# Kernel tuning notes

Measured on AMD Instinct MI355X. Metric: run time of the kernel, lower is better.

Reference implementation:

```python
import jax, jax.numpy as jnp
import numpy as np

D = 2048
N = 16384
ETA = 0.01


def setup_inputs() -> dict:
    key = jax.random.key(0)
    k_theta, k_xs = jax.random.split(key)
    theta = jax.random.normal(k_theta, (D,), dtype=jnp.float32)
    # per-layer params x_k, init uniform(-1/sqrt(d), 1/sqrt(d)) as in torch module
    stdv = 1.0 / np.sqrt(D)
    xs = jax.random.uniform(k_xs, (N, D), dtype=jnp.float32, minval=-stdv, maxval=stdv)
    return {"theta": theta, "xs": xs}


def reference(theta, xs):
    # Each layer: pred = <x, theta>; grad = -x / (1 + exp(pred));
    # theta_next = theta - eta * grad = theta + eta * x / (1 + exp(pred)).
    def step(th, x):
        pred = jnp.dot(x, th)
        th_next = th + ETA * x / (1.0 + jnp.exp(pred))
        return th_next, None

    theta_out, _ = jax.lax.scan(step, theta, xs)
    return theta_out
```

## Files before the change

kernel.cpp:

```cpp
#include <hip/hip_runtime.h>
#include <hip/hip_bf16.h>
#include <stdint.h>

#define D_DIM 2048
#define N_STEPS 16384
#define B_BLK 1024
#define N_BLK (N_STEPS / B_BLK)
#define T_P (B_BLK / 128)
#define N_TILE (T_P * (T_P + 1) / 2)
#define ETA 0.01f
#define NWG 256
#define FLAG_STRIDE 16
#define FLAG_INTS (NWG * FLAG_STRIDE + 16)

typedef __attribute__((ext_vector_type(8))) short short8_t;
typedef __attribute__((ext_vector_type(4))) float floatx4;

__device__ __forceinline__ short f2bf(float f) {
  __hip_bfloat16 h = __float2bfloat16(f);
  return __builtin_bit_cast(short, h);
}
__device__ __forceinline__ float bf2f(uint32_t bits) {
  return __builtin_bit_cast(float, bits << 16);
}

__device__ __forceinline__ void store_wt(float* p, float v) {
  __hip_atomic_store(p, v, __ATOMIC_RELAXED, __HIP_MEMORY_SCOPE_AGENT);
}

__device__ __forceinline__ void gl_lds16(const short* g, short* l) {
  __builtin_amdgcn_global_load_lds(
      (const __attribute__((address_space(1))) void*)g,
      (__attribute__((address_space(3))) void*)l, 16, 0, 0);
}

__global__ __launch_bounds__(256) void cast_kernel(
    const float* __restrict__ xs, short* __restrict__ xb,
    const float* __restrict__ theta_in, float* __restrict__ theta_arr,
    int* __restrict__ flags) {
  size_t i = (size_t)blockIdx.x * 256 + threadIdx.x;
  float4 a = ((const float4*)xs)[i * 2];
  float4 b = ((const float4*)xs)[i * 2 + 1];
  short8_t v;
  v[0] = f2bf(a.x); v[1] = f2bf(a.y); v[2] = f2bf(a.z); v[3] = f2bf(a.w);
  v[4] = f2bf(b.x); v[5] = f2bf(b.y); v[6] = f2bf(b.z); v[7] = f2bf(b.w);
  *(short8_t*)(xb + i * 8) = v;

  if (blockIdx.x == 0) {
    int tid = threadIdx.x;
    for (int k = tid; k < FLAG_INTS; k += 256) flags[k] = 0;
    float4 t0 = ((const float4*)theta_in)[tid * 2];
    float4 t1 = ((const float4*)theta_in)[tid * 2 + 1];
    ((float4*)theta_arr)[tid * 2] = t0;
    ((float4*)theta_arr)[tid * 2 + 1] = t1;
  }
}

__global__ __launch_bounds__(256) void gram_kernel(const short* __restrict__ xb,
                                                   short* __restrict__ G) {
  int i = blockIdx.x;
  int x = i & 7, j = i >> 3;
  int b = (j < 36) ? x : x + 8;
  int t = (j < 36) ? j : j - 36;
  int ti = 0;
  while ((ti + 1) * (ti + 2) / 2 <= t) ti++;
  int tj = t - ti * (ti + 1) / 2;

  __shared__ short As[128 * 64];
  __shared__ short Bs[128 * 64];

  int tid = threadIdx.x;
  int lane = tid & 63;
  int w = tid >> 6;
  int wm = w >> 1, wn = w & 1;
  int quad = lane >> 4, rr = lane & 15;

  floatx4 acc[4][4];
#pragma unroll
  for (int ii = 0; ii < 4; ii++)
#pragma unroll
    for (int jj = 0; jj < 4; jj++)
#pragma unroll
      for (int r = 0; r < 4; r++) acc[ii][jj][r] = 0.f;

  const short* Arow = xb + (size_t)(b * B_BLK + ti * 128) * D_DIM;
  const short* Brow = xb + (size_t)(b * B_BLK + tj * 128) * D_DIM;
  bool diag = (ti == tj);

  for (int kk = 0; kk < D_DIM; kk += 64) {
#pragma unroll
    for (int tch = 0; tch < 4; tch++) {
      int chunk = tch * 256 + tid;
      int row = chunk >> 3, slot = chunk & 7;
      int cc = slot ^ (row & 7);
      gl_lds16(Arow + (size_t)row * D_DIM + kk + cc * 8, &As[chunk * 8]);
      if (!diag)
        gl_lds16(Brow + (size_t)row * D_DIM + kk + cc * 8, &Bs[chunk * 8]);
    }
    __syncthreads();

    const short* Bsrc = diag ? As : Bs;
#pragma unroll
    for (int ks = 0; ks < 2; ks++) {
      short8_t af[4], bfr[4];
#pragma unroll
      for (int mt = 0; mt < 4; mt++) {
        int r = wm * 64 + mt * 16 + rr;
        int slot = (ks * 4 + quad) ^ (r & 7);
        af[mt] = *(const short8_t*)(&As[r * 64 + slot * 8]);
      }
#pragma unroll
      for (int nt = 0; nt < 4; nt++) {
        int r = wn * 64 + nt * 16 + rr;
        int slot = (ks * 4 + quad) ^ (r & 7);
        bfr[nt] = *(const short8_t*)(&Bsrc[r * 64 + slot * 8]);
      }
#pragma unroll
      for (int mt = 0; mt < 4; mt++)
#pragma unroll
        for (int nt = 0; nt < 4; nt++)
          acc[mt][nt] = __builtin_amdgcn_mfma_f32_16x16x32_bf16(
              af[mt], bfr[nt], acc[mt][nt], 0, 0, 0);
    }
    __syncthreads();
  }

  size_t gbase = ((size_t)(b * N_TILE + t)) * (128 * 128);
  int col0 = lane & 15;
  int row0 = (lane >> 4) * 4;
#pragma unroll
  for (int mt = 0; mt < 4; mt++)
#pragma unroll
    for (int nt = 0; nt < 4; nt++)
#pragma unroll
      for (int r = 0; r < 4; r++) {
        int row = wm * 64 + mt * 16 + row0 + r;
        int col = wn * 64 + nt * 16 + col0;
        G[gbase + (size_t)row * 128 + col] = f2bf(acc[mt][nt][r]);
      }
}

__device__ __forceinline__ void bar_arrive(int* flags, int wg, int tid,
                                           int gen) {
  __syncthreads();
  if (tid == 0)
    __hip_atomic_store(&flags[wg * FLAG_STRIDE], gen, __ATOMIC_RELAXED,
                       __HIP_MEMORY_SCOPE_AGENT);
}

__device__ __forceinline__ void bar_wait(int* flags, int tid, int gen) {
  int guard = 0;
  while (__hip_atomic_load(&flags[tid * FLAG_STRIDE], __ATOMIC_RELAXED,
                           __HIP_MEMORY_SCOPE_AGENT) < gen &&
         guard < (1 << 20)) {
    guard++;
    __builtin_amdgcn_s_sleep(1);
  }
  asm volatile("" ::: "memory");
  __syncthreads();
}

__device__ __forceinline__ float wave_reduce(float s) {
  for (int off = 32; off; off >>= 1) s += __shfl_xor(s, off, 64);
  return s;
}

__global__ __launch_bounds__(256, 1) void solve_kernel(
    const short* __restrict__ xb, const short* __restrict__ G,
    float* __restrict__ theta_arr, float* __restrict__ c0_arr,
    float* __restrict__ c1_arr, int* flags, float* __restrict__ d_out) {
  int tid = threadIdx.x;
  int wg = blockIdx.x;
  int lane = tid & 63;
  int wid = tid >> 6;
  int gw = wg * 4 + wid;
  int ti = gw >> 7, kr = gw & 127;
  int oct = (wg & 7) * 32 + (wg >> 3);
  int d0 = oct * 8;
  int gen = 0;

  __shared__ float redc[4][8];

  short8_t xa[4];
  uint32_t gv[8];
  short8_t xc[4];

  {
    const short* xr = xb + (size_t)gw * D_DIM;
#pragma unroll
    for (int i = 0; i < 4; i++)
      xa[i] = *(const short8_t*)(xr + (i * 64 + lane) * 8);
#pragma unroll
    for (int tj = 0; tj < T_P; tj++)
      if (tj <= ti) {
        size_t base = ((size_t)(ti * (ti + 1) / 2 + tj)) * (128 * 128) +
                      (size_t)kr * 128;
        gv[tj] = *(const uint32_t*)(G + base + lane * 2);
      }
  }

  for (int b = 0; b < N_BLK; b++) {
    const float* theta = theta_arr + (size_t)b * D_DIM;
    float* c0 = c0_arr + (size_t)b * B_BLK;
    float* c1 = c1_arr + (size_t)b * B_BLK;
    float p_k;
    float th8 = 0.f;

    {
      if (tid < 8) th8 = theta[d0 + tid];
      float s = 0.f;
#pragma unroll
      for (int i = 0; i < 4; i++) {
        int idx = (i * 64 + lane) * 8;
        float4 t0 = *(const float4*)(theta + idx);
        float4 t1 = *(const float4*)(theta + idx + 4);
        short8_t xv = xa[i];
        s += bf2f((uint16_t)xv[0]) * t0.x + bf2f((uint16_t)xv[1]) * t0.y +
             bf2f((uint16_t)xv[2]) * t0.z + bf2f((uint16_t)xv[3]) * t0.w +
             bf2f((uint16_t)xv[4]) * t1.x + bf2f((uint16_t)xv[5]) * t1.y +
             bf2f((uint16_t)xv[6]) * t1.z + bf2f((uint16_t)xv[7]) * t1.w;
      }
      s = wave_reduce(s);
      p_k = s;
      if (lane == 0) store_wt(&c0[gw], ETA / (1.f + __expf(s)));
    }
    bar_arrive(flags, wg, tid, ++gen);
    {
      const short* xp = xb + ((size_t)b * B_BLK + tid * 4) * D_DIM + d0;
#pragma unroll
      for (int j = 0; j < 4; j++)
        xc[j] = *(const short8_t*)(xp + (size_t)j * D_DIM);
    }
    bar_wait(flags, tid, gen);

    {
      float2 cv[T_P];
#pragma unroll
      for (int tj = 0; tj < T_P; tj++)
        if (tj <= ti) cv[tj] = *(const float2*)(c0 + tj * 128 + lane * 2);
      float s = 0.f;
      int jc = lane * 2;
#pragma unroll
      for (int tj = 0; tj < T_P; tj++)
        if (tj <= ti) {
          int lim = (tj == ti) ? kr : 128;
          if (jc < lim) s += bf2f(gv[tj] & 0xffffu) * cv[tj].x;
          if (jc + 1 < lim) s += bf2f(gv[tj] >> 16) * cv[tj].y;
        }
      s = wave_reduce(s);
      if (lane == 0) store_wt(&c1[gw], ETA / (1.f + __expf(p_k + s)));
    }
    bar_arrive(flags, wg, tid, ++gen);
    if (b + 1 < N_BLK) {
      const short* xr = xb + (size_t)((b + 1) * B_BLK + gw) * D_DIM;
#pragma unroll
      for (int i = 0; i < 4; i++)
        xa[i] = *(const short8_t*)(xr + (i * 64 + lane) * 8);
    }
    bar_wait(flags, tid, gen);

    {
      float4 c1v = *(const float4*)(c1 + tid * 4);
      float a8[8];
#pragma unroll
      for (int jj = 0; jj < 8; jj++) a8[jj] = 0.f;
#pragma unroll
      for (int j = 0; j < 4; j++) {
        float c = (&c1v.x)[j];
        short8_t xv = xc[j];
#pragma unroll
        for (int jj = 0; jj < 8; jj++) a8[jj] += c * bf2f((uint16_t)xv[jj]);
      }
#pragma unroll
      for (int off = 32; off; off >>= 1)
#pragma unroll
        for (int jj = 0; jj < 8; jj++) a8[jj] += __shfl_xor(a8[jj], off, 64);
      if (lane == 0) {
#pragma unroll
        for (int jj = 0; jj < 8; jj++) redc[wid][jj] = a8[jj];
      }
      __syncthreads();
      if (tid < 8) {
        float tot =
            redc[0][tid] + redc[1][tid] + redc[2][tid] + redc[3][tid];
        float* dst = (b + 1 < N_BLK)
                         ? &theta_arr[(size_t)(b + 1) * D_DIM + d0 + tid]
                         : &d_out[d0 + tid];
        store_wt(dst, th8 + tot);
      }
    }
    if (b + 1 < N_BLK) {
      bar_arrive(flags, wg, tid, ++gen);
      {
        size_t base =
            ((size_t)((b + 1) * N_TILE + ti * (ti + 1) / 2)) * (128 * 128) +
            (size_t)kr * 128;
#pragma unroll
        for (int tj = 0; tj < T_P; tj++)
          if (tj <= ti)
            gv[tj] = *(const uint32_t*)(G + base + (size_t)tj * (128 * 128) +
                                        lane * 2);
      }
      bar_wait(flags, tid, gen);
    }
  }
}

extern "C" void kernel_launch(void* const* d_in, const int* in_sizes, int n_in,
                              void* d_out, int out_size, void* d_ws,
                              size_t ws_size, hipStream_t stream) {
  const float* theta_in = (const float*)d_in[0];
  const float* xs = (const float*)d_in[1];

  char* ws = (char*)d_ws;
  const size_t XB_BYTES = (size_t)N_STEPS * D_DIM * sizeof(short);
  const size_t G_BYTES = (size_t)N_BLK * N_TILE * 128 * 128 * sizeof(short);
  short* xb = (short*)ws;
  short* G = (short*)(ws + XB_BYTES);
  float* theta_arr = (float*)(ws + XB_BYTES + G_BYTES);
  float* c0_arr = theta_arr + (size_t)(N_BLK + 1) * D_DIM;
  float* c1_arr = c0_arr + (size_t)N_BLK * B_BLK;
  int* flags = (int*)(c1_arr + (size_t)N_BLK * B_BLK);

  cast_kernel<<<(N_STEPS * D_DIM / 8) / 256, 256, 0, stream>>>(
      xs, xb, theta_in, theta_arr, flags);
  gram_kernel<<<N_BLK * N_TILE, 256, 0, stream>>>(xb, G);
  solve_kernel<<<NWG, 256, 0, stream>>>(xb, G, theta_arr, c0_arr, c1_arr,
                                        flags, (float*)d_out);
}
```

Measured before the change: 350.7 us.

## Fuse cast and Gram into one prep kernel with per-block readiness counters

The separate cast and Gram kernels are merged into a single prep kernel. Cast workgroups (one per row) write bf16 rows and bump a per-block counter, and Gram workgroups spin until their block's rows are ready, so Gram work can overlap the cast instead of waiting for a full kernel boundary. Flag initialisation moves to a hipMemsetAsync. The solve kernel is split into two launches over halves of the blocks, with the barrier generation carried across. This relies on cast workgroups being scheduled ahead of the spinning Gram workgroups and adds an extra launch and a memset.

```diff
diff --git a/kernel.cpp b/kernel.cpp
--- a/kernel.cpp
+++ b/kernel.cpp
@@ -12,9 +12,13 @@
 #define NWG 256
 #define FLAG_STRIDE 16
 #define FLAG_INTS (NWG * FLAG_STRIDE + 16)
+#define GRAM_WGS (N_BLK * N_TILE)
+#define CAST_WGS N_STEPS
+#define PREP_WGS (GRAM_WGS + CAST_WGS)
 
 typedef __attribute__((ext_vector_type(8))) short short8_t;
 typedef __attribute__((ext_vector_type(4))) float floatx4;
+typedef __attribute__((ext_vector_type(2))) unsigned long long ulong2_t;
 
 __device__ __forceinline__ short f2bf(float f) {
   __hip_bfloat16 h = __float2bfloat16(f);
@@ -25,6 +29,9 @@
 }
 
 __device__ __forceinline__ void store_wt(float* p, float v) {
+  __hip_atomic_store(p, v, __ATOMIC_RELAXED, __HIP_MEMORY_SCOPE_AGENT);
+}
+__device__ __forceinline__ void store_wt64(uint64_t* p, uint64_t v) {
   __hip_atomic_store(p, v, __ATOMIC_RELAXED, __HIP_MEMORY_SCOPE_AGENT);
 }
 
@@ -34,42 +41,58 @@
       (__attribute__((address_space(3))) void*)l, 16, 0, 0);
 }
 
-__global__ __launch_bounds__(256) void cast_kernel(
-    const float* __restrict__ xs, short* __restrict__ xb,
+__global__ __launch_bounds__(256) void prep_kernel(
+    const float* __restrict__ xs, short* xb, short* __restrict__ G,
     const float* __restrict__ theta_in, float* __restrict__ theta_arr,
-    int* __restrict__ flags) {
-  size_t i = (size_t)blockIdx.x * 256 + threadIdx.x;
-  float4 a = ((const float4*)xs)[i * 2];
-  float4 b = ((const float4*)xs)[i * 2 + 1];
-  short8_t v;
-  v[0] = f2bf(a.x); v[1] = f2bf(a.y); v[2] = f2bf(a.z); v[3] = f2bf(a.w);
-  v[4] = f2bf(b.x); v[5] = f2bf(b.y); v[6] = f2bf(b.z); v[7] = f2bf(b.w);
-  *(short8_t*)(xb + i * 8) = v;
-
-  if (blockIdx.x == 0) {
-    int tid = threadIdx.x;
-    for (int k = tid; k < FLAG_INTS; k += 256) flags[k] = 0;
-    float4 t0 = ((const float4*)theta_in)[tid * 2];
-    float4 t1 = ((const float4*)theta_in)[tid * 2 + 1];
-    ((float4*)theta_arr)[tid * 2] = t0;
-    ((float4*)theta_arr)[tid * 2 + 1] = t1;
-  }
-}
-
-__global__ __launch_bounds__(256) void gram_kernel(const short* __restrict__ xb,
-                                                   short* __restrict__ G) {
-  int i = blockIdx.x;
-  int x = i & 7, j = i >> 3;
-  int b = (j < 36) ? x : x + 8;
-  int t = (j < 36) ? j : j - 36;
+    int* castcnt) {
+  int tid = threadIdx.x;
+  int wg = blockIdx.x;
+
+  __shared__ short As[128 * 64];
+  __shared__ short Bs[128 * 64];
+
+  if (wg >= GRAM_WGS) {
+    int r = wg - GRAM_WGS;
+    const float* src = xs + (size_t)r * D_DIM + tid * 8;
+    float4 a = *(const float4*)(src);
+    float4 bq = *(const float4*)(src + 4);
+    short8_t v;
+    v[0] = f2bf(a.x); v[1] = f2bf(a.y); v[2] = f2bf(a.z); v[3] = f2bf(a.w);
+    v[4] = f2bf(bq.x); v[5] = f2bf(bq.y); v[6] = f2bf(bq.z); v[7] = f2bf(bq.w);
+    ulong2_t u = __builtin_bit_cast(ulong2_t, v);
+    uint64_t* dst = (uint64_t*)(xb + (size_t)r * D_DIM + tid * 8);
+    store_wt64(dst, u[0]);
+    store_wt64(dst + 1, u[1]);
+    __syncthreads();
+    if (tid == 0)
+      __hip_atomic_fetch_add(&castcnt[(r >> 10) * FLAG_STRIDE], 1,
+                             __ATOMIC_RELAXED, __HIP_MEMORY_SCOPE_AGENT);
+    if (r == 0) {
+      float4 t0 = ((const float4*)theta_in)[tid * 2];
+      float4 t1 = ((const float4*)theta_in)[tid * 2 + 1];
+      ((float4*)theta_arr)[tid * 2] = t0;
+      ((float4*)theta_arr)[tid * 2 + 1] = t1;
+    }
+    return;
+  }
+
+  int b = wg / N_TILE, t = wg % N_TILE;
   int ti = 0;
   while ((ti + 1) * (ti + 2) / 2 <= t) ti++;
   int tj = t - ti * (ti + 1) / 2;
 
-  __shared__ short As[128 * 64];
-  __shared__ short Bs[128 * 64];
-
-  int tid = threadIdx.x;
+  if (tid == 0) {
+    int guard = 0;
+    while (__hip_atomic_load(&castcnt[b * FLAG_STRIDE], __ATOMIC_RELAXED,
+                             __HIP_MEMORY_SCOPE_AGENT) < B_BLK &&
+           guard < (1 << 22)) {
+      guard++;
+      __builtin_amdgcn_s_sleep(2);
+    }
+  }
+  __syncthreads();
+  asm volatile("" ::: "memory");
+
   int lane = tid & 63;
   int w = tid >> 6;
   int wm = w >> 1, wn = w & 1;
@@ -168,7 +191,8 @@
 __global__ __launch_bounds__(256, 1) void solve_kernel(
     const short* __restrict__ xb, const short* __restrict__ G,
     float* __restrict__ theta_arr, float* __restrict__ c0_arr,
-    float* __restrict__ c1_arr, int* flags, float* __restrict__ d_out) {
+    float* __restrict__ c1_arr, int* flags, float* __restrict__ d_out,
+    int b0, int b1, int gen0) {
   int tid = threadIdx.x;
   int wg = blockIdx.x;
   int lane = tid & 63;
@@ -177,7 +201,7 @@
   int ti = gw >> 7, kr = gw & 127;
   int oct = (wg & 7) * 32 + (wg >> 3);
   int d0 = oct * 8;
-  int gen = 0;
+  int gen = gen0;
 
   __shared__ float redc[4][8];
 
@@ -186,20 +210,21 @@
   short8_t xc[4];
 
   {
-    const short* xr = xb + (size_t)gw * D_DIM;
+    const short* xr = xb + (size_t)(b0 * B_BLK + gw) * D_DIM;
 #pragma unroll
     for (int i = 0; i < 4; i++)
       xa[i] = *(const short8_t*)(xr + (i * 64 + lane) * 8);
 #pragma unroll
     for (int tj = 0; tj < T_P; tj++)
       if (tj <= ti) {
-        size_t base = ((size_t)(ti * (ti + 1) / 2 + tj)) * (128 * 128) +
-                      (size_t)kr * 128;
+        size_t base =
+            ((size_t)(b0 * N_TILE + ti * (ti + 1) / 2 + tj)) * (128 * 128) +
+            (size_t)kr * 128;
         gv[tj] = *(const uint32_t*)(G + base + lane * 2);
       }
   }
 
-  for (int b = 0; b < N_BLK; b++) {
+  for (int b = b0; b < b1; b++) {
     const float* theta = theta_arr + (size_t)b * D_DIM;
     float* c0 = c0_arr + (size_t)b * B_BLK;
     float* c1 = c1_arr + (size_t)b * B_BLK;
@@ -251,7 +276,7 @@
       if (lane == 0) store_wt(&c1[gw], ETA / (1.f + __expf(p_k + s)));
     }
     bar_arrive(flags, wg, tid, ++gen);
-    if (b + 1 < N_BLK) {
+    if (b + 1 < b1) {
       const short* xr = xb + (size_t)((b + 1) * B_BLK + gw) * D_DIM;
 #pragma unroll
       for (int i = 0; i < 4; i++)
@@ -289,7 +314,7 @@
         store_wt(dst, th8 + tot);
       }
     }
-    if (b + 1 < N_BLK) {
+    if (b + 1 < b1) {
       bar_arrive(flags, wg, tid, ++gen);
       {
         size_t base =
@@ -321,10 +346,15 @@
   float* c0_arr = theta_arr + (size_t)(N_BLK + 1) * D_DIM;
   float* c1_arr = c0_arr + (size_t)N_BLK * B_BLK;
   int* flags = (int*)(c1_arr + (size_t)N_BLK * B_BLK);
-
-  cast_kernel<<<(N_STEPS * D_DIM / 8) / 256, 256, 0, stream>>>(
-      xs, xb, theta_in, theta_arr, flags);
-  gram_kernel<<<N_BLK * N_TILE, 256, 0, stream>>>(xb, G);
+  int* castcnt = flags + FLAG_INTS;
+
+  hipMemsetAsync(flags, 0, (FLAG_INTS + N_BLK * FLAG_STRIDE) * sizeof(int),
+                 stream);
+  prep_kernel<<<PREP_WGS, 256, 0, stream>>>(xs, xb, G, theta_in, theta_arr,
+                                            castcnt);
   solve_kernel<<<NWG, 256, 0, stream>>>(xb, G, theta_arr, c0_arr, c1_arr,
-                                        flags, (float*)d_out);
-}
+                                        flags, (float*)d_out, 0, N_BLK / 2, 0);
+  solve_kernel<<<NWG, 256, 0, stream>>>(xb, G, theta_arr, c0_arr, c1_arr,
+                                        flags, (float*)d_out, N_BLK / 2, N_BLK,
+                                        23);
+}
```

Result: slower. 868.9 us (+147.7%).
